# Optimization experiments

Measured on AMD Instinct MI355X. Metric: run time of the kernel, lower is better.

Reference implementation:

```python
import jax, jax.numpy as jnp
import numpy as np

N = 200000   # total nodes across batched graphs
E = 800000   # directed edges (grid graph, avg degree ~4)
G = 8        # number of graphs in the batch
IN_DIM, INTER_DIM, OUT_DIM, LAYER_NUM = 2, 128, 64, 4


def setup_inputs() -> dict:
    key = jax.random.key(0)
    ks = jax.random.split(key, 10)
    x = jax.random.normal(ks[0], (N, IN_DIM), jnp.float32)
    edge_index = jax.random.randint(ks[1], (2, E), 0, N, dtype=jnp.int32)
    batch = jnp.sort(jax.random.randint(ks[2], (N,), 0, G, dtype=jnp.int32))

    def glorot(k, fan_in, fan_out):
        s = (2.0 / (fan_in + fan_out)) ** 0.5
        return jax.random.normal(k, (fan_in, fan_out), jnp.float32) * s

    W_in = glorot(ks[3], IN_DIM, INTER_DIM)
    b_in = jnp.zeros((INTER_DIM,), jnp.float32)
    W_hidden = jnp.stack([glorot(jax.random.fold_in(ks[4], i), INTER_DIM, INTER_DIM)
                          for i in range(LAYER_NUM)])
    b_hidden = jnp.zeros((LAYER_NUM, INTER_DIM), jnp.float32)
    W_out = glorot(ks[5], INTER_DIM, OUT_DIM)
    b_out = jnp.zeros((OUT_DIM,), jnp.float32)
    return {"x": x, "edge_index": edge_index, "batch": batch,
            "W_in": W_in, "b_in": b_in, "W_hidden": W_hidden,
            "b_hidden": b_hidden, "W_out": W_out, "b_out": b_out}


def reference(x, edge_index, batch, W_in, b_in, W_hidden, b_hidden, W_out, b_out):
    num_nodes = x.shape[0]
    loops = jnp.arange(num_nodes, dtype=edge_index.dtype)
    # PyG GCNConv: add self loops, symmetric degree normalization
    src = jnp.concatenate([edge_index[0], loops])
    dst = jnp.concatenate([edge_index[1], loops])
    deg = jax.ops.segment_sum(jnp.ones_like(src, x.dtype), dst, num_segments=num_nodes)
    dinv = jnp.where(deg > 0, jax.lax.rsqrt(jnp.maximum(deg, 1.0)), 0.0)
    norm = dinv[src] * dinv[dst]  # [E+N]

    def gcn_conv(h, W, b):
        m = h @ W                                  # [N, F'] dense transform
        msg = norm[:, None] * m[src]               # gather + scale
        out = jax.ops.segment_sum(msg, dst, num_segments=num_nodes)  # scatter-add
        return out + b

    h = gcn_conv(x, W_in, b_in)
    for i in range(W_hidden.shape[0]):
        h = jax.nn.relu(gcn_conv(h, W_hidden[i], b_hidden[i]))
    h = gcn_conv(h, W_out, b_out)

    # global mean pool over batch assignment, then sigmoid
    sums = jax.ops.segment_sum(h, batch, num_segments=G)
    cnts = jax.ops.segment_sum(jnp.ones((num_nodes,), h.dtype), batch, num_segments=G)
    return jax.nn.sigmoid(sums / jnp.maximum(cnts, 1.0)[:, None])
```

## Files before the change

kernel.cpp:

```cpp
#include <hip/hip_runtime.h>
#include <math.h>

#define INTER 128
#define OUTD  64
#define SCAN_T 256
#define SCAN_E 1024
#define NSLOT 64
#define NBIN  128

using bf16x8 = __attribute__((ext_vector_type(8))) short;
using f32x4  = __attribute__((ext_vector_type(4))) float;

static __device__ __forceinline__ unsigned short f2bf(float f) {
    unsigned int u = __float_as_uint(f);
    u += 0x7fffu + ((u >> 16) & 1u);
    return (unsigned short)(u >> 16);
}
static __device__ __forceinline__ unsigned int pk2(float a, float b) {
    return (unsigned int)f2bf(a) | ((unsigned int)f2bf(b) << 16);
}
static __device__ __forceinline__ float bflo(unsigned int u) { return __uint_as_float(u << 16); }
static __device__ __forceinline__ float bfhi(unsigned int u) { return __uint_as_float(u & 0xffff0000u); }

static __device__ __forceinline__ void fma8(float* a, float w, uint4 v) {
    a[0] = fmaf(w, bflo(v.x), a[0]); a[1] = fmaf(w, bfhi(v.x), a[1]);
    a[2] = fmaf(w, bflo(v.y), a[2]); a[3] = fmaf(w, bfhi(v.y), a[3]);
    a[4] = fmaf(w, bflo(v.z), a[4]); a[5] = fmaf(w, bfhi(v.z), a[5]);
    a[6] = fmaf(w, bflo(v.w), a[6]); a[7] = fmaf(w, bfhi(v.w), a[7]);
}
static __device__ __forceinline__ void seed8(float* a, float sn, uint4 v) {
    a[0] = sn * bflo(v.x); a[1] = sn * bfhi(v.x);
    a[2] = sn * bflo(v.y); a[3] = sn * bfhi(v.y);
    a[4] = sn * bflo(v.z); a[5] = sn * bfhi(v.z);
    a[6] = sn * bflo(v.w); a[7] = sn * bfhi(v.w);
}

__global__ void count_k(const int* __restrict__ dst, int* __restrict__ cnt, int E) {
    int e = blockIdx.x * 256 + threadIdx.x;
    if (e < E) atomicAdd(&cnt[dst[e]], 1);
}

__global__ void dinv_k(const int* __restrict__ cnt, float* __restrict__ dinv, int N) {
    int i = blockIdx.x * 256 + threadIdx.x;
    if (i < N) dinv[i] = rsqrtf((float)(cnt[i] + 1));
}

__global__ void scan_block(const int* __restrict__ in, int* __restrict__ out,
                           int* __restrict__ bsums, int n) {
    __shared__ int sh[SCAN_T];
    int base = blockIdx.x * SCAN_E;
    int t = threadIdx.x;
    int v[4];
    int s = 0;
#pragma unroll
    for (int i = 0; i < 4; i++) {
        int idx = base + t * 4 + i;
        v[i] = (idx < n) ? in[idx] : 0;
        s += v[i];
    }
    sh[t] = s;
    __syncthreads();
    for (int off = 1; off < SCAN_T; off <<= 1) {
        int x = (t >= off) ? sh[t - off] : 0;
        __syncthreads();
        sh[t] += x;
        __syncthreads();
    }
    int excl = (t == 0) ? 0 : sh[t - 1];
    if (bsums && t == SCAN_T - 1) bsums[blockIdx.x] = sh[t];
#pragma unroll
    for (int i = 0; i < 4; i++) {
        int idx = base + t * 4 + i;
        if (idx < n) out[idx] = excl;
        excl += v[i];
    }
}

__global__ void scan_add(int* __restrict__ out, const int* __restrict__ bsums, int n, int total) {
    int idx = blockIdx.x * SCAN_E + threadIdx.x * 4;
    int add = bsums[blockIdx.x];
#pragma unroll
    for (int i = 0; i < 4; i++) {
        int j = idx + i;
        if (j < n) out[j] += add;
    }
    if (blockIdx.x == 0 && threadIdx.x == 0) out[n] = total;
}

__global__ void scatter_k(const int* __restrict__ src, const int* __restrict__ dst,
                          const int* __restrict__ rs, int* __restrict__ cursor,
                          const float* __restrict__ dinv,
                          int2* __restrict__ cw, int E) {
    int e = blockIdx.x * 256 + threadIdx.x;
    if (e >= E) return;
    int s = src[e], d = dst[e];
    int pos = rs[d] + atomicAdd(&cursor[d], 1);
    cw[pos] = make_int2(s, __float_as_int(dinv[s] * dinv[d]));
}

__global__ __launch_bounds__(256) void dhist2_k(const int* __restrict__ cnt,
                                                int* __restrict__ blockhist,
                                                int N, int nblk) {
    __shared__ int hist[NBIN];
    int t = threadIdx.x;
    if (t < NBIN) hist[t] = 0;
    __syncthreads();
    int i = blockIdx.x * 256 + t;
    if (i < N) atomicAdd(&hist[min(cnt[i], NBIN - 1)], 1);
    __syncthreads();
    if (t < NBIN) blockhist[t * nblk + blockIdx.x] = hist[t];
}

__global__ __launch_bounds__(256) void dorder2_k(const int* __restrict__ cnt,
                                                 const int* __restrict__ offs,
                                                 int* __restrict__ order,
                                                 int N, int nblk) {
    __shared__ int cur[NBIN];
    int t = threadIdx.x;
    if (t < NBIN) cur[t] = 0;
    __syncthreads();
    int i = blockIdx.x * 256 + t;
    if (i >= N) return;
    int d = min(cnt[i], NBIN - 1);
    int r = atomicAdd(&cur[d], 1);
    order[offs[d * nblk + blockIdx.x] + r] = i;
}

__global__ void wprep_h(const float* __restrict__ W, unsigned short* __restrict__ Wt, int L) {
    int tid = blockIdx.x * 256 + threadIdx.x;
    if (tid >= L * INTER * INTER) return;
    int l = tid / (INTER * INTER);
    int r = tid % (INTER * INTER);
    int n = r / INTER, k = r % INTER;
    Wt[tid] = f2bf(W[(size_t)l * INTER * INTER + (size_t)k * INTER + n]);
}

__global__ void wprep_o(const float* __restrict__ W, unsigned short* __restrict__ Wt) {
    int tid = blockIdx.x * 256 + threadIdx.x;
    if (tid >= OUTD * INTER) return;
    int n = tid / INTER, k = tid % INTER;
    Wt[tid] = f2bf(W[(size_t)k * OUTD + n]);
}

__global__ void agg2(const float* __restrict__ x, const int* __restrict__ rs,
                     const int2* __restrict__ cw, const float* __restrict__ dinv,
                     float* __restrict__ ax, int N) {
    int i = blockIdx.x * 256 + threadIdx.x;
    if (i >= N) return;
    float di = dinv[i];
    float sn = di * di;
    float2 xv = ((const float2*)x)[i];
    float a0 = sn * xv.x, a1 = sn * xv.y;
    int e0 = rs[i], e1 = rs[i + 1];
    for (int k = e0; k < e1; k++) {
        int2 c = cw[k];
        float wk = __int_as_float(c.y);
        float2 xs = ((const float2*)x)[c.x];
        a0 += wk * xs.x;
        a1 += wk * xs.y;
    }
    ((float2*)ax)[i] = make_float2(a0, a1);
}

__global__ void gemm_in(const float* __restrict__ ax, const float* __restrict__ Wi,
                        const float* __restrict__ bi, unsigned short* __restrict__ h, int N) {
    int node = blockIdx.x * 2 + threadIdx.x / 128;
    int j = threadIdx.x % 128;
    if (node >= N) return;
    float2 a = ((const float2*)ax)[node];
    h[(size_t)node * 128 + j] = f2bf(fmaf(a.x, Wi[j], fmaf(a.y, Wi[128 + j], bi[j])));
}

__global__ __launch_bounds__(256) void fused_hidden4(
    const unsigned short* __restrict__ Hin,
    const int* __restrict__ rs, const int2* __restrict__ cw,
    const float* __restrict__ dinv, const int* __restrict__ order,
    const unsigned short* __restrict__ Wt,
    const float* __restrict__ bias,
    unsigned short* __restrict__ Hout, int N)
{
    __shared__ __align__(16) unsigned short T[32][136];
    __shared__ int nodeid[32];
    const int t = threadIdx.x;
    const int q = t & 15;
    const int gi = t >> 4;
    const int sA = blockIdx.x * 32 + gi;
    const int sB = sA + 16;
    const bool vA = sA < N, vB = sB < N;
    const int nA = vA ? order[sA] : 0;
    const int nB = vB ? order[sB] : 0;
    if (q == 0) {
        nodeid[gi]      = vA ? nA : -1;
        nodeid[gi + 16] = vB ? nB : -1;
    }

    float accA[8] = {0,0,0,0,0,0,0,0}, accB[8] = {0,0,0,0,0,0,0,0};
    if (vA) {
        float dA = dinv[nA];
        seed8(accA, dA * dA, *(const uint4*)(Hin + (size_t)nA * 128 + q * 8));
    }
    if (vB) {
        float dB = dinv[nB];
        seed8(accB, dB * dB, *(const uint4*)(Hin + (size_t)nB * 128 + q * 8));
    }
    int kA = 0, eA = 0, kB = 0, eB = 0;
    if (vA) { kA = rs[nA]; eA = rs[nA + 1]; }
    if (vB) { kB = rs[nB]; eB = rs[nB + 1]; }

    while (kA < eA || kB < eB) {
        int2 cA0 = (kA     < eA) ? cw[kA]     : make_int2(0, 0);
        int2 cA1 = (kA + 1 < eA) ? cw[kA + 1] : make_int2(0, 0);
        int2 cA2 = (kA + 2 < eA) ? cw[kA + 2] : make_int2(0, 0);
        int2 cA3 = (kA + 3 < eA) ? cw[kA + 3] : make_int2(0, 0);
        int2 cB0 = (kB     < eB) ? cw[kB]     : make_int2(0, 0);
        int2 cB1 = (kB + 1 < eB) ? cw[kB + 1] : make_int2(0, 0);
        int2 cB2 = (kB + 2 < eB) ? cw[kB + 2] : make_int2(0, 0);
        int2 cB3 = (kB + 3 < eB) ? cw[kB + 3] : make_int2(0, 0);
        uint4 vA0 = *(const uint4*)(Hin + (size_t)cA0.x * 128 + q * 8);
        uint4 vA1 = *(const uint4*)(Hin + (size_t)cA1.x * 128 + q * 8);
        uint4 vA2 = *(const uint4*)(Hin + (size_t)cA2.x * 128 + q * 8);
        uint4 vA3 = *(const uint4*)(Hin + (size_t)cA3.x * 128 + q * 8);
        uint4 vB0 = *(const uint4*)(Hin + (size_t)cB0.x * 128 + q * 8);
        uint4 vB1 = *(const uint4*)(Hin + (size_t)cB1.x * 128 + q * 8);
        uint4 vB2 = *(const uint4*)(Hin + (size_t)cB2.x * 128 + q * 8);
        uint4 vB3 = *(const uint4*)(Hin + (size_t)cB3.x * 128 + q * 8);
        fma8(accA, __int_as_float(cA0.y), vA0);
        fma8(accA, __int_as_float(cA1.y), vA1);
        fma8(accA, __int_as_float(cA2.y), vA2);
        fma8(accA, __int_as_float(cA3.y), vA3);
        fma8(accB, __int_as_float(cB0.y), vB0);
        fma8(accB, __int_as_float(cB1.y), vB1);
        fma8(accB, __int_as_float(cB2.y), vB2);
        fma8(accB, __int_as_float(cB3.y), vB3);
        kA += 4; kB += 4;
    }

    {
        uint4 oA = make_uint4(pk2(accA[0], accA[1]), pk2(accA[2], accA[3]),
                              pk2(accA[4], accA[5]), pk2(accA[6], accA[7]));
        uint4 oB = make_uint4(pk2(accB[0], accB[1]), pk2(accB[2], accB[3]),
                              pk2(accB[4], accB[5]), pk2(accB[6], accB[7]));
        *(uint4*)&T[gi][q * 8] = oA;
        *(uint4*)&T[gi + 16][q * 8] = oB;
    }
    __syncthreads();

    const int wv = t >> 6;
    const int lane = t & 63;
    const int r15 = lane & 15;
    const int kg = lane >> 4;

    bf16x8 bfr[2][4];
#pragma unroll
    for (int nc = 0; nc < 2; nc++)
#pragma unroll
        for (int ks = 0; ks < 4; ks++)
            bfr[nc][ks] = *(const bf16x8*)&T[nc * 16 + r15][kg * 8 + ks * 32];

    f32x4 acc[2][2];
#pragma unroll
    for (int nc = 0; nc < 2; nc++)
#pragma unroll
        for (int c = 0; c < 2; c++) acc[nc][c] = (f32x4){0.f, 0.f, 0.f, 0.f};

#pragma unroll
    for (int c = 0; c < 2; c++) {
        const unsigned short* wrow = Wt + (size_t)(wv * 32 + c * 16 + r15) * 128 + kg * 8;
#pragma unroll
        for (int ks = 0; ks < 4; ks++) {
            bf16x8 afr = *(const bf16x8*)(wrow + ks * 32);
            acc[0][c] = __builtin_amdgcn_mfma_f32_16x16x32_bf16(afr, bfr[0][ks], acc[0][c], 0, 0, 0);
            acc[1][c] = __builtin_amdgcn_mfma_f32_16x16x32_bf16(afr, bfr[1][ks], acc[1][c], 0, 0, 0);
        }
    }

#pragma unroll
    for (int nc = 0; nc < 2; nc++) {
        const int node = nodeid[nc * 16 + r15];
        if (node >= 0) {
#pragma unroll
            for (int c = 0; c < 2; c++) {
                int col = wv * 32 + c * 16 + kg * 4;
                float4 bv = *(const float4*)(bias + col);
                float v0 = fmaxf(acc[nc][c][0] + bv.x, 0.f);
                float v1 = fmaxf(acc[nc][c][1] + bv.y, 0.f);
                float v2 = fmaxf(acc[nc][c][2] + bv.z, 0.f);
                float v3 = fmaxf(acc[nc][c][3] + bv.w, 0.f);
                *(uint2*)(Hout + (size_t)node * 128 + col) = make_uint2(pk2(v0, v1), pk2(v2, v3));
            }
        }
    }
}

__global__ __launch_bounds__(256) void gemm_out(const unsigned short* __restrict__ Hin,
                                                const unsigned short* __restrict__ Wt,
                                                unsigned short* __restrict__ g, int N) {
    const int wv = threadIdx.x >> 6;
    const int lane = threadIdx.x & 63;
    const int r15 = lane & 15;
    const int kg = lane >> 4;
    const int node0 = blockIdx.x * 64 + wv * 16;
    if (node0 >= N) return;

    int arow = node0 + r15;
    if (arow >= N) arow = N - 1;
    bf16x8 bfr[4];
#pragma unroll
    for (int ks = 0; ks < 4; ks++)
        bfr[ks] = __builtin_nontemporal_load(
            (const bf16x8*)(Hin + (size_t)arow * 128 + kg * 8 + ks * 32));

    f32x4 acc[4];
#pragma unroll
    for (int c = 0; c < 4; c++) acc[c] = (f32x4){0.f, 0.f, 0.f, 0.f};

#pragma unroll
    for (int c = 0; c < 4; c++) {
        const unsigned short* wrow = Wt + (size_t)(c * 16 + r15) * 128 + kg * 8;
#pragma unroll
        for (int ks = 0; ks < 4; ks++) {
            bf16x8 afr = *(const bf16x8*)(wrow + ks * 32);
            acc[c] = __builtin_amdgcn_mfma_f32_16x16x32_bf16(afr, bfr[ks], acc[c], 0, 0, 0);
        }
    }
    const int node = node0 + r15;
    if (node < N) {
#pragma unroll
        for (int c = 0; c < 4; c++) {
            int col = c * 16 + kg * 4;
            *(uint2*)(g + (size_t)node * 64 + col) =
                make_uint2(pk2(acc[c][0], acc[c][1]), pk2(acc[c][2], acc[c][3]));
        }
    }
}

__global__ __launch_bounds__(256) void fused_last2(
    const unsigned short* __restrict__ g,
    const int* __restrict__ rs, const int2* __restrict__ cw,
    const float* __restrict__ dinv, const int* __restrict__ batch,
    float* __restrict__ gsum , int N)
{
    __shared__ __align__(16) float R[64][68];
    __shared__ int gid[64];
    const int t = threadIdx.x;
    const int q = t & 7;
    const int gi = t >> 3;
    const int nA = blockIdx.x * 64 + gi;
    const int nB = nA + 32;
    const bool vA = nA < N, vB = nB < N;

    float accA[8] = {0,0,0,0,0,0,0,0}, accB[8] = {0,0,0,0,0,0,0,0};
    if (vA) {
        float dA = dinv[nA];
        seed8(accA, dA * dA, *(const uint4*)(g + (size_t)nA * 64 + q * 8));
    }
    if (vB) {
        float dB = dinv[nB];
        seed8(accB, dB * dB, *(const uint4*)(g + (size_t)nB * 64 + q * 8));
    }
    int kA = 0, eA = 0, kB = 0, eB = 0;
    if (vA) { kA = rs[nA]; eA = rs[nA + 1]; }
    if (vB) { kB = rs[nB]; eB = rs[nB + 1]; }

    while (kA < eA || kB < eB) {
        int2 cA0 = (kA     < eA) ? cw[kA]     : make_int2(0, 0);
        int2 cA1 = (kA + 1 < eA) ? cw[kA + 1] : make_int2(0, 0);
        int2 cA2 = (kA + 2 < eA) ? cw[kA + 2] : make_int2(0, 0);
        int2 cA3 = (kA + 3 < eA) ? cw[kA + 3] : make_int2(0, 0);
        int2 cB0 = (kB     < eB) ? cw[kB]     : make_int2(0, 0);
        int2 cB1 = (kB + 1 < eB) ? cw[kB + 1] : make_int2(0, 0);
        int2 cB2 = (kB + 2 < eB) ? cw[kB + 2] : make_int2(0, 0);
        int2 cB3 = (kB + 3 < eB) ? cw[kB + 3] : make_int2(0, 0);
        uint4 vA0 = *(const uint4*)(g + (size_t)cA0.x * 64 + q * 8);
        uint4 vA1 = *(const uint4*)(g + (size_t)cA1.x * 64 + q * 8);
        uint4 vA2 = *(const uint4*)(g + (size_t)cA2.x * 64 + q * 8);
        uint4 vA3 = *(const uint4*)(g + (size_t)cA3.x * 64 + q * 8);
        uint4 vB0 = *(const uint4*)(g + (size_t)cB0.x * 64 + q * 8);
        uint4 vB1 = *(const uint4*)(g + (size_t)cB1.x * 64 + q * 8);
        uint4 vB2 = *(const uint4*)(g + (size_t)cB2.x * 64 + q * 8);
        uint4 vB3 = *(const uint4*)(g + (size_t)cB3.x * 64 + q * 8);
        fma8(accA, __int_as_float(cA0.y), vA0);
        fma8(accA, __int_as_float(cA1.y), vA1);
        fma8(accA, __int_as_float(cA2.y), vA2);
        fma8(accA, __int_as_float(cA3.y), vA3);
        fma8(accB, __int_as_float(cB0.y), vB0);
        fma8(accB, __int_as_float(cB1.y), vB1);
        fma8(accB, __int_as_float(cB2.y), vB2);
        fma8(accB, __int_as_float(cB3.y), vB3);
        kA += 4; kB += 4;
    }

#pragma unroll
    for (int j = 0; j < 8; j += 4) {
        *(float4*)&R[gi][q * 8 + j]      = make_float4(accA[j], accA[j+1], accA[j+2], accA[j+3]);
        *(float4*)&R[gi + 32][q * 8 + j] = make_float4(accB[j], accB[j+1], accB[j+2], accB[j+3]);
    }
    if (q == 0) {
        gid[gi]      = vA ? batch[nA] : -1;
        gid[gi + 32] = vB ? batch[nB] : -1;
    }
    __syncthreads();

    const int f = t & 63;
    const int half = t >> 6;
    const int slot = blockIdx.x & (NSLOT - 1);
    float acc = 0.f;
    int cur = -1;
    for (int r = 0; r < 16; r++) {
        int row = half * 16 + r;
        int gg = gid[row];
        if (gg != cur) {
            if (cur >= 0) atomicAdd(&gsum[(size_t)(slot * 8 + cur) * 64 + f], acc);
            acc = 0.f; cur = gg;
        }
        if (gg >= 0) acc += R[row][f];
    }
    if (cur >= 0) atomicAdd(&gsum[(size_t)(slot * 8 + cur) * 64 + f], acc);
}

__global__ void gbound_k(const int* __restrict__ batch, int* __restrict__ gstart, int N, int G) {
    int i = blockIdx.x * 256 + threadIdx.x;
    if (i >= N) return;
    int b = batch[i];
    int prev = (i == 0) ? -1 : batch[i - 1];
    for (int g = prev + 1; g <= b; g++) gstart[g] = i;
    if (i == N - 1) for (int g = b + 1; g <= G; g++) gstart[g] = N;
}

__global__ void final4_k(const float* __restrict__ gsum, const int* __restrict__ gstart,
                         const float* __restrict__ b_out, float* __restrict__ out) {
    int t = threadIdx.x;
    int g = t >> 6, f = t & 63;
    float s = 0.f;
    for (int sl = 0; sl < NSLOT; sl++) s += gsum[(size_t)(sl * 8 + g) * 64 + f];
    int c = gstart[g + 1] - gstart[g];
    float v = s / (float)max(c, 1) + b_out[f];
    out[g * 64 + f] = 1.f / (1.f + expf(-v));
}

extern "C" void kernel_launch(void* const* d_in, const int* in_sizes, int n_in,
                              void* d_out, int out_size, void* d_ws, size_t ws_size,
                              hipStream_t stream) {
    const float* x     = (const float*)d_in[0];
    const int*   ei    = (const int*)d_in[1];
    const int*   batch = (const int*)d_in[2];
    const float* W_in  = (const float*)d_in[3];
    const float* b_in  = (const float*)d_in[4];
    const float* W_h   = (const float*)d_in[5];
    const float* b_h   = (const float*)d_in[6];
    const float* W_out = (const float*)d_in[7];
    const float* b_out = (const float*)d_in[8];

    const int N = in_sizes[2];
    const int E = in_sizes[1] / 2;
    const int L = in_sizes[5] / (INTER * INTER);
    const int G = 8;
    const int* src = ei;
    const int* dst = ei + E;
    const int nblk = (N + 255) / 256;
    const int nbh = NBIN * nblk;

    char* ws = (char*)d_ws;
    size_t off = 0;
    auto alloc = [&](size_t bytes) -> void* {
        void* p = ws + off;
        off += (bytes + 255) & ~(size_t)255;
        return p;
    };
    int*   cnt    = (int*)alloc((size_t)N * 4);
    int*   cursor = (int*)alloc((size_t)N * 4);
    int*   rs     = (int*)alloc((size_t)(N + 1) * 4);
    int*   bsums  = (int*)alloc(4096);
    float* dinv   = (float*)alloc((size_t)N * 4);
    int2*  cw     = (int2*)alloc((size_t)E * 8);
    float* ax     = (float*)alloc((size_t)N * 2 * 4);
    unsigned short* h   = (unsigned short*)alloc((size_t)N * INTER * 2);
    unsigned short* h2  = (unsigned short*)alloc((size_t)N * INTER * 2);
    unsigned short* g   = (unsigned short*)alloc((size_t)N * OUTD * 2);
    unsigned short* Wht = (unsigned short*)alloc((size_t)L * INTER * INTER * 2);
    unsigned short* Wot = (unsigned short*)alloc((size_t)OUTD * INTER * 2);
    float* gsum   = (float*)alloc((size_t)NSLOT * 8 * OUTD * 4);
    int*   gstart = (int*)alloc((G + 1) * 4);
    int*   bh     = (int*)alloc((size_t)(nbh + 1) * 4);
    int*   order  = (int*)alloc((size_t)N * 4);
    (void)ws_size; (void)n_in;

    hipMemsetAsync(cnt, 0, (size_t)N * 4, stream);
    hipMemsetAsync(cursor, 0, (size_t)N * 4, stream);
    hipMemsetAsync(gsum, 0, (size_t)NSLOT * 8 * OUTD * 4, stream);

    count_k<<<(E + 255) / 256, 256, 0, stream>>>(dst, cnt, E);
    dinv_k<<<nblk, 256, 0, stream>>>(cnt, dinv, N);
    int nsb = (N + SCAN_E - 1) / SCAN_E;
    scan_block<<<nsb, SCAN_T, 0, stream>>>(cnt, rs, bsums, N);
    scan_block<<<1, SCAN_T, 0, stream>>>(bsums, bsums, nullptr, nsb);
    scan_add<<<nsb, SCAN_T, 0, stream>>>(rs, bsums, N, E);
    scatter_k<<<(E + 255) / 256, 256, 0, stream>>>(src, dst, rs, cursor, dinv, cw, E);
    gbound_k<<<nblk, 256, 0, stream>>>(batch, gstart, N, G);

    dhist2_k<<<nblk, 256, 0, stream>>>(cnt, bh, N, nblk);
    int nsb2 = (nbh + SCAN_E - 1) / SCAN_E;
    scan_block<<<nsb2, SCAN_T, 0, stream>>>(bh, bh, bsums, nbh);
    scan_block<<<1, SCAN_T, 0, stream>>>(bsums, bsums, nullptr, nsb2);
    scan_add<<<nsb2, SCAN_T, 0, stream>>>(bh, bsums, nbh, N);
    dorder2_k<<<nblk, 256, 0, stream>>>(cnt, bh, order, N, nblk);

    wprep_h<<<(L * INTER * INTER + 255) / 256, 256, 0, stream>>>(W_h, Wht, L);
    wprep_o<<<(OUTD * INTER + 255) / 256, 256, 0, stream>>>(W_out, Wot);

    agg2<<<nblk, 256, 0, stream>>>(x, rs, cw, dinv, ax, N);
    gemm_in<<<(N + 1) / 2, 256, 0, stream>>>(ax, W_in, b_in, h, N);

    unsigned short* hin = h;
    unsigned short* hout = h2;
    for (int l = 0; l < L; l++) {
        fused_hidden4<<<(N + 31) / 32, 256, 0, stream>>>(
            hin, rs, cw, dinv, order, Wht + (size_t)l * INTER * INTER, b_h + (size_t)l * INTER, hout, N);
        unsigned short* tmp = hin; hin = hout; hout = tmp;
    }

    gemm_out<<<(N + 63) / 64, 256, 0, stream>>>(hin, Wot, g, N);
    fused_last2<<<(N + 63) / 64, 256, 0, stream>>>(g, rs, cw, dinv, batch, gsum, N);
    final4_k<<<1, 512, 0, stream>>>(gsum, gstart, b_out, (float*)d_out);
}
```

Before: 542.9 us.

## Fuse preprocessing kernels, pack per-node metadata, sort by graph and degree, deepen gather unroll

Merges dinv, graph-boundary and histogram kernels into one prep kernel, merges both weight-prep kernels, and fuses the input aggregation with the input linear layer. Nodes are now sorted by (graph, capped degree) into an int4 record holding node id, row range and dinv, so the hidden and last layers read one record instead of several scattered lookups. The hidden-layer gather unroll is raised from 4 to 8 edges per iteration for more memory-level parallelism, at the cost of more registers. The last layer now walks sorted order, which should make its pooled rows more graph-coherent. The two count/cursor memsets are merged into one, which assumes cursor sits right after cnt.

```diff
diff --git a/kernel.cpp b/kernel.cpp
--- a/kernel.cpp
+++ b/kernel.cpp
@@ -6,7 +6,7 @@
 #define SCAN_T 256
 #define SCAN_E 1024
 #define NSLOT 64
-#define NBIN  128
+#define NBIN  256
 
 using bf16x8 = __attribute__((ext_vector_type(8))) short;
 using f32x4  = __attribute__((ext_vector_type(4))) float;
@@ -38,11 +38,6 @@
 __global__ void count_k(const int* __restrict__ dst, int* __restrict__ cnt, int E) {
     int e = blockIdx.x * 256 + threadIdx.x;
     if (e < E) atomicAdd(&cnt[dst[e]], 1);
-}
-
-__global__ void dinv_k(const int* __restrict__ cnt, float* __restrict__ dinv, int N) {
-    int i = blockIdx.x * 256 + threadIdx.x;
-    if (i < N) dinv[i] = rsqrtf((float)(cnt[i] + 1));
 }
 
 __global__ void scan_block(const int* __restrict__ in, int* __restrict__ out,
@@ -98,22 +93,36 @@
     cw[pos] = make_int2(s, __float_as_int(dinv[s] * dinv[d]));
 }
 
-__global__ __launch_bounds__(256) void dhist2_k(const int* __restrict__ cnt,
-                                                int* __restrict__ blockhist,
-                                                int N, int nblk) {
+__global__ __launch_bounds__(256) void prep2_k(const int* __restrict__ cnt,
+                                               const int* __restrict__ batch,
+                                               float* __restrict__ dinv,
+                                               int* __restrict__ blockhist,
+                                               int* __restrict__ gstart,
+                                               int N, int G, int nblk) {
     __shared__ int hist[NBIN];
     int t = threadIdx.x;
     if (t < NBIN) hist[t] = 0;
     __syncthreads();
     int i = blockIdx.x * 256 + t;
-    if (i < N) atomicAdd(&hist[min(cnt[i], NBIN - 1)], 1);
+    if (i < N) {
+        int d = cnt[i];
+        dinv[i] = rsqrtf((float)(d + 1));
+        int b = batch[i];
+        atomicAdd(&hist[b * 32 + min(d, 31)], 1);
+        int prev = (i == 0) ? -1 : batch[i - 1];
+        for (int g2 = prev + 1; g2 <= b; g2++) gstart[g2] = i;
+        if (i == N - 1) for (int g2 = b + 1; g2 <= G; g2++) gstart[g2] = N;
+    }
     __syncthreads();
     if (t < NBIN) blockhist[t * nblk + blockIdx.x] = hist[t];
 }
 
-__global__ __launch_bounds__(256) void dorder2_k(const int* __restrict__ cnt,
+__global__ __launch_bounds__(256) void dorder3_k(const int* __restrict__ cnt,
+                                                 const int* __restrict__ batch,
+                                                 const int* __restrict__ rs,
+                                                 const float* __restrict__ dinv,
                                                  const int* __restrict__ offs,
-                                                 int* __restrict__ order,
+                                                 int4* __restrict__ srt,
                                                  int N, int nblk) {
     __shared__ int cur[NBIN];
     int t = threadIdx.x;
@@ -121,60 +130,87 @@
     __syncthreads();
     int i = blockIdx.x * 256 + t;
     if (i >= N) return;
-    int d = min(cnt[i], NBIN - 1);
-    int r = atomicAdd(&cur[d], 1);
-    order[offs[d * nblk + blockIdx.x] + r] = i;
-}
-
-__global__ void wprep_h(const float* __restrict__ W, unsigned short* __restrict__ Wt, int L) {
+    int key = batch[i] * 32 + min(cnt[i], 31);
+    int r = atomicAdd(&cur[key], 1);
+    int p = offs[key * nblk + blockIdx.x] + r;
+    srt[p] = make_int4(i, rs[i], rs[i + 1], __float_as_int(dinv[i]));
+}
+
+__global__ void wprep_all(const float* __restrict__ Wh, const float* __restrict__ Wo,
+                          unsigned short* __restrict__ Wht, unsigned short* __restrict__ Wot,
+                          int L) {
     int tid = blockIdx.x * 256 + threadIdx.x;
-    if (tid >= L * INTER * INTER) return;
-    int l = tid / (INTER * INTER);
-    int r = tid % (INTER * INTER);
-    int n = r / INTER, k = r % INTER;
-    Wt[tid] = f2bf(W[(size_t)l * INTER * INTER + (size_t)k * INTER + n]);
-}
-
-__global__ void wprep_o(const float* __restrict__ W, unsigned short* __restrict__ Wt) {
-    int tid = blockIdx.x * 256 + threadIdx.x;
-    if (tid >= OUTD * INTER) return;
-    int n = tid / INTER, k = tid % INTER;
-    Wt[tid] = f2bf(W[(size_t)k * OUTD + n]);
-}
-
-__global__ void agg2(const float* __restrict__ x, const int* __restrict__ rs,
-                     const int2* __restrict__ cw, const float* __restrict__ dinv,
-                     float* __restrict__ ax, int N) {
-    int i = blockIdx.x * 256 + threadIdx.x;
-    if (i >= N) return;
-    float di = dinv[i];
-    float sn = di * di;
-    float2 xv = ((const float2*)x)[i];
-    float a0 = sn * xv.x, a1 = sn * xv.y;
-    int e0 = rs[i], e1 = rs[i + 1];
-    for (int k = e0; k < e1; k++) {
-        int2 c = cw[k];
-        float wk = __int_as_float(c.y);
-        float2 xs = ((const float2*)x)[c.x];
-        a0 += wk * xs.x;
-        a1 += wk * xs.y;
-    }
-    ((float2*)ax)[i] = make_float2(a0, a1);
-}
-
-__global__ void gemm_in(const float* __restrict__ ax, const float* __restrict__ Wi,
-                        const float* __restrict__ bi, unsigned short* __restrict__ h, int N) {
-    int node = blockIdx.x * 2 + threadIdx.x / 128;
-    int j = threadIdx.x % 128;
-    if (node >= N) return;
-    float2 a = ((const float2*)ax)[node];
-    h[(size_t)node * 128 + j] = f2bf(fmaf(a.x, Wi[j], fmaf(a.y, Wi[128 + j], bi[j])));
-}
-
-__global__ __launch_bounds__(256) void fused_hidden4(
+    int nh = L * INTER * INTER;
+    if (tid < nh) {
+        int l = tid / (INTER * INTER);
+        int r = tid % (INTER * INTER);
+        int n = r / INTER, k = r % INTER;
+        Wht[tid] = f2bf(Wh[(size_t)l * INTER * INTER + (size_t)k * INTER + n]);
+    } else if (tid < nh + OUTD * INTER) {
+        int r = tid - nh;
+        int n = r / INTER, k = r % INTER;
+        Wot[r] = f2bf(Wo[(size_t)k * OUTD + n]);
+    }
+}
+
+__global__ __launch_bounds__(256) void agg_in_k(const float* __restrict__ x,
+                                                const int* __restrict__ rs,
+                                                const int2* __restrict__ cw,
+                                                const float* __restrict__ dinv,
+                                                const float* __restrict__ Wi,
+                                                const float* __restrict__ bi,
+                                                unsigned short* __restrict__ h, int N) {
+    __shared__ float2 axs[256];
+    int t = threadIdx.x;
+    int i = blockIdx.x * 256 + t;
+    float a0 = 0.f, a1 = 0.f;
+    if (i < N) {
+        float di = dinv[i];
+        float sn = di * di;
+        float2 xv = ((const float2*)x)[i];
+        a0 = sn * xv.x; a1 = sn * xv.y;
+        int e0 = rs[i], e1 = rs[i + 1];
+        for (int k = e0; k < e1; k += 2) {
+            int2 c0 = cw[k];
+            int2 c1 = (k + 1 < e1) ? cw[k + 1] : make_int2(0, 0);
+            float2 x0 = ((const float2*)x)[c0.x];
+            float2 x1 = ((const float2*)x)[c1.x];
+            float w0 = __int_as_float(c0.y), w1 = __int_as_float(c1.y);
+            a0 = fmaf(w0, x0.x, a0); a1 = fmaf(w0, x0.y, a1);
+            a0 = fmaf(w1, x1.x, a0); a1 = fmaf(w1, x1.y, a1);
+        }
+    }
+    axs[t] = make_float2(a0, a1);
+    __syncthreads();
+    int base = blockIdx.x * 256;
+#pragma unroll
+    for (int p = 0; p < 16; p++) {
+        int nl = p * 16 + (t >> 4);
+        int nb = base + nl;
+        if (nb < N) {
+            int j0 = (t & 15) * 8;
+            float2 a = axs[nl];
+            float4 wa0 = *(const float4*)&Wi[j0];       float4 wa1 = *(const float4*)&Wi[j0 + 4];
+            float4 wb0 = *(const float4*)&Wi[128 + j0]; float4 wb1 = *(const float4*)&Wi[128 + j0 + 4];
+            float4 bb0 = *(const float4*)&bi[j0];       float4 bb1 = *(const float4*)&bi[j0 + 4];
+            float h0 = fmaf(a.x, wa0.x, fmaf(a.y, wb0.x, bb0.x));
+            float h1 = fmaf(a.x, wa0.y, fmaf(a.y, wb0.y, bb0.y));
+            float h2 = fmaf(a.x, wa0.z, fmaf(a.y, wb0.z, bb0.z));
+            float h3 = fmaf(a.x, wa0.w, fmaf(a.y, wb0.w, bb0.w));
+            float h4 = fmaf(a.x, wa1.x, fmaf(a.y, wb1.x, bb1.x));
+            float h5 = fmaf(a.x, wa1.y, fmaf(a.y, wb1.y, bb1.y));
+            float h6 = fmaf(a.x, wa1.z, fmaf(a.y, wb1.z, bb1.z));
+            float h7 = fmaf(a.x, wa1.w, fmaf(a.y, wb1.w, bb1.w));
+            *(uint4*)(h + (size_t)nb * 128 + j0) =
+                make_uint4(pk2(h0, h1), pk2(h2, h3), pk2(h4, h5), pk2(h6, h7));
+        }
+    }
+}
+
+__global__ __launch_bounds__(256) void fused_hidden6(
     const unsigned short* __restrict__ Hin,
-    const int* __restrict__ rs, const int2* __restrict__ cw,
-    const float* __restrict__ dinv, const int* __restrict__ order,
+    const int2* __restrict__ cw,
+    const int4* __restrict__ srt,
     const unsigned short* __restrict__ Wt,
     const float* __restrict__ bias,
     unsigned short* __restrict__ Hout, int N)
@@ -186,53 +222,45 @@
     const int gi = t >> 4;
     const int sA = blockIdx.x * 32 + gi;
     const int sB = sA + 16;
-    const bool vA = sA < N, vB = sB < N;
-    const int nA = vA ? order[sA] : 0;
-    const int nB = vB ? order[sB] : 0;
+    int4 dA = (sA < N) ? srt[sA] : make_int4(-1, 0, 0, 0);
+    int4 dB = (sB < N) ? srt[sB] : make_int4(-1, 0, 0, 0);
     if (q == 0) {
-        nodeid[gi]      = vA ? nA : -1;
-        nodeid[gi + 16] = vB ? nB : -1;
+        nodeid[gi]      = dA.x;
+        nodeid[gi + 16] = dB.x;
     }
 
     float accA[8] = {0,0,0,0,0,0,0,0}, accB[8] = {0,0,0,0,0,0,0,0};
-    if (vA) {
-        float dA = dinv[nA];
-        seed8(accA, dA * dA, *(const uint4*)(Hin + (size_t)nA * 128 + q * 8));
-    }
-    if (vB) {
-        float dB = dinv[nB];
-        seed8(accB, dB * dB, *(const uint4*)(Hin + (size_t)nB * 128 + q * 8));
-    }
     int kA = 0, eA = 0, kB = 0, eB = 0;
-    if (vA) { kA = rs[nA]; eA = rs[nA + 1]; }
-    if (vB) { kB = rs[nB]; eB = rs[nB + 1]; }
+    if (dA.x >= 0) {
+        float dv = __int_as_float(dA.w);
+        seed8(accA, dv * dv, *(const uint4*)(Hin + (size_t)dA.x * 128 + q * 8));
+        kA = dA.y; eA = dA.z;
+    }
+    if (dB.x >= 0) {
+        float dv = __int_as_float(dB.w);
+        seed8(accB, dv * dv, *(const uint4*)(Hin + (size_t)dB.x * 128 + q * 8));
+        kB = dB.y; eB = dB.z;
+    }
 
     while (kA < eA || kB < eB) {
-        int2 cA0 = (kA     < eA) ? cw[kA]     : make_int2(0, 0);
-        int2 cA1 = (kA + 1 < eA) ? cw[kA + 1] : make_int2(0, 0);
-        int2 cA2 = (kA + 2 < eA) ? cw[kA + 2] : make_int2(0, 0);
-        int2 cA3 = (kA + 3 < eA) ? cw[kA + 3] : make_int2(0, 0);
-        int2 cB0 = (kB     < eB) ? cw[kB]     : make_int2(0, 0);
-        int2 cB1 = (kB + 1 < eB) ? cw[kB + 1] : make_int2(0, 0);
-        int2 cB2 = (kB + 2 < eB) ? cw[kB + 2] : make_int2(0, 0);
-        int2 cB3 = (kB + 3 < eB) ? cw[kB + 3] : make_int2(0, 0);
-        uint4 vA0 = *(const uint4*)(Hin + (size_t)cA0.x * 128 + q * 8);
-        uint4 vA1 = *(const uint4*)(Hin + (size_t)cA1.x * 128 + q * 8);
-        uint4 vA2 = *(const uint4*)(Hin + (size_t)cA2.x * 128 + q * 8);
-        uint4 vA3 = *(const uint4*)(Hin + (size_t)cA3.x * 128 + q * 8);
-        uint4 vB0 = *(const uint4*)(Hin + (size_t)cB0.x * 128 + q * 8);
-        uint4 vB1 = *(const uint4*)(Hin + (size_t)cB1.x * 128 + q * 8);
-        uint4 vB2 = *(const uint4*)(Hin + (size_t)cB2.x * 128 + q * 8);
-        uint4 vB3 = *(const uint4*)(Hin + (size_t)cB3.x * 128 + q * 8);
-        fma8(accA, __int_as_float(cA0.y), vA0);
-        fma8(accA, __int_as_float(cA1.y), vA1);
-        fma8(accA, __int_as_float(cA2.y), vA2);
-        fma8(accA, __int_as_float(cA3.y), vA3);
-        fma8(accB, __int_as_float(cB0.y), vB0);
-        fma8(accB, __int_as_float(cB1.y), vB1);
-        fma8(accB, __int_as_float(cB2.y), vB2);
-        fma8(accB, __int_as_float(cB3.y), vB3);
-        kA += 4; kB += 4;
+        int2 cA[8], cB[8];
+#pragma unroll
+        for (int u = 0; u < 8; u++) {
+            cA[u] = (kA + u < eA) ? cw[kA + u] : make_int2(0, 0);
+            cB[u] = (kB + u < eB) ? cw[kB + u] : make_int2(0, 0);
+        }
+        uint4 vA[8], vB[8];
+#pragma unroll
+        for (int u = 0; u < 8; u++) {
+            vA[u] = *(const uint4*)(Hin + (size_t)cA[u].x * 128 + q * 8);
+            vB[u] = *(const uint4*)(Hin + (size_t)cB[u].x * 128 + q * 8);
+        }
+#pragma unroll
+        for (int u = 0; u < 8; u++) {
+            fma8(accA, __int_as_float(cA[u].y), vA[u]);
+            fma8(accB, __int_as_float(cB[u].y), vB[u]);
+        }
+        kA += 8; kB += 8;
     }
 
     {
@@ -334,10 +362,11 @@
     }
 }
 
-__global__ __launch_bounds__(256) void fused_last2(
+__global__ __launch_bounds__(256) void fused_last3(
     const unsigned short* __restrict__ g,
-    const int* __restrict__ rs, const int2* __restrict__ cw,
-    const float* __restrict__ dinv, const int* __restrict__ batch,
+    const int2* __restrict__ cw,
+    const int4* __restrict__ srt,
+    const int* __restrict__ batch,
     float* __restrict__ gsum , int N)
 {
     __shared__ __align__(16) float R[64][68];
@@ -345,48 +374,46 @@
     const int t = threadIdx.x;
     const int q = t & 7;
     const int gi = t >> 3;
-    const int nA = blockIdx.x * 64 + gi;
-    const int nB = nA + 32;
-    const bool vA = nA < N, vB = nB < N;
+    const int sA = blockIdx.x * 64 + gi;
+    const int sB = sA + 32;
+    int4 dA = (sA < N) ? srt[sA] : make_int4(-1, 0, 0, 0);
+    int4 dB = (sB < N) ? srt[sB] : make_int4(-1, 0, 0, 0);
+    if (q == 0) {
+        gid[gi]      = (dA.x >= 0) ? batch[dA.x] : -1;
+        gid[gi + 32] = (dB.x >= 0) ? batch[dB.x] : -1;
+    }
 
     float accA[8] = {0,0,0,0,0,0,0,0}, accB[8] = {0,0,0,0,0,0,0,0};
-    if (vA) {
-        float dA = dinv[nA];
-        seed8(accA, dA * dA, *(const uint4*)(g + (size_t)nA * 64 + q * 8));
-    }
-    if (vB) {
-        float dB = dinv[nB];
-        seed8(accB, dB * dB, *(const uint4*)(g + (size_t)nB * 64 + q * 8));
-    }
     int kA = 0, eA = 0, kB = 0, eB = 0;
-    if (vA) { kA = rs[nA]; eA = rs[nA + 1]; }
-    if (vB) { kB = rs[nB]; eB = rs[nB + 1]; }
+    if (dA.x >= 0) {
+        float dv = __int_as_float(dA.w);
+        seed8(accA, dv * dv, *(const uint4*)(g + (size_t)dA.x * 64 + q * 8));
+        kA = dA.y; eA = dA.z;
+    }
+    if (dB.x >= 0) {
+        float dv = __int_as_float(dB.w);
+        seed8(accB, dv * dv, *(const uint4*)(g + (size_t)dB.x * 64 + q * 8));
+        kB = dB.y; eB = dB.z;
+    }
 
     while (kA < eA || kB < eB) {
-        int2 cA0 = (kA     < eA) ? cw[kA]     : make_int2(0, 0);
-        int2 cA1 = (kA + 1 < eA) ? cw[kA + 1] : make_int2(0, 0);
-        int2 cA2 = (kA + 2 < eA) ? cw[kA + 2] : make_int2(0, 0);
-        int2 cA3 = (kA + 3 < eA) ? cw[kA + 3] : make_int2(0, 0);
-        int2 cB0 = (kB     < eB) ? cw[kB]     : make_int2(0, 0);
-        int2 cB1 = (kB + 1 < eB) ? cw[kB + 1] : make_int2(0, 0);
-        int2 cB2 = (kB + 2 < eB) ? cw[kB + 2] : make_int2(0, 0);
-        int2 cB3 = (kB + 3 < eB) ? cw[kB + 3] : make_int2(0, 0);
-        uint4 vA0 = *(const uint4*)(g + (size_t)cA0.x * 64 + q * 8);
-        uint4 vA1 = *(const uint4*)(g + (size_t)cA1.x * 64 + q * 8);
-        uint4 vA2 = *(const uint4*)(g + (size_t)cA2.x * 64 + q * 8);
-        uint4 vA3 = *(const uint4*)(g + (size_t)cA3.x * 64 + q * 8);
-        uint4 vB0 = *(const uint4*)(g + (size_t)cB0.x * 64 + q * 8);
-        uint4 vB1 = *(const uint4*)(g + (size_t)cB1.x * 64 + q * 8);
-        uint4 vB2 = *(const uint4*)(g + (size_t)cB2.x * 64 + q * 8);
-        uint4 vB3 = *(const uint4*)(g + (size_t)cB3.x * 64 + q * 8);
-        fma8(accA, __int_as_float(cA0.y), vA0);
-        fma8(accA, __int_as_float(cA1.y), vA1);
-        fma8(accA, __int_as_float(cA2.y), vA2);
-        fma8(accA, __int_as_float(cA3.y), vA3);
-        fma8(accB, __int_as_float(cB0.y), vB0);
-        fma8(accB, __int_as_float(cB1.y), vB1);
-        fma8(accB, __int_as_float(cB2.y), vB2);
-        fma8(accB, __int_as_float(cB3.y), vB3);
+        int2 cA[4], cB[4];
+#pragma unroll
+        for (int u = 0; u < 4; u++) {
+            cA[u] = (kA + u < eA) ? cw[kA + u] : make_int2(0, 0);
+            cB[u] = (kB + u < eB) ? cw[kB + u] : make_int2(0, 0);
+        }
+        uint4 vA[4], vB[4];
+#pragma unroll
+        for (int u = 0; u < 4; u++) {
+            vA[u] = *(const uint4*)(g + (size_t)cA[u].x * 64 + q * 8);
+            vB[u] = *(const uint4*)(g + (size_t)cB[u].x * 64 + q * 8);
+        }
+#pragma unroll
+        for (int u = 0; u < 4; u++) {
+            fma8(accA, __int_as_float(cA[u].y), vA[u]);
+            fma8(accB, __int_as_float(cB[u].y), vB[u]);
+        }
         kA += 4; kB += 4;
     }
 
@@ -394,10 +421,6 @@
     for (int j = 0; j < 8; j += 4) {
         *(float4*)&R[gi][q * 8 + j]      = make_float4(accA[j], accA[j+1], accA[j+2], accA[j+3]);
         *(float4*)&R[gi + 32][q * 8 + j] = make_float4(accB[j], accB[j+1], accB[j+2], accB[j+3]);
-    }
-    if (q == 0) {
-        gid[gi]      = vA ? batch[nA] : -1;
-        gid[gi + 32] = vB ? batch[nB] : -1;
     }
     __syncthreads();
 
@@ -416,15 +439,6 @@
         if (gg >= 0) acc += R[row][f];
     }
     if (cur >= 0) atomicAdd(&gsum[(size_t)(slot * 8 + cur) * 64 + f], acc);
-}
-
-__global__ void gbound_k(const int* __restrict__ batch, int* __restrict__ gstart, int N, int G) {
-    int i = blockIdx.x * 256 + threadIdx.x;
-    if (i >= N) return;
-    int b = batch[i];
-    int prev = (i == 0) ? -1 : batch[i - 1];
-    for (int g = prev + 1; g <= b; g++) gstart[g] = i;
-    if (i == N - 1) for (int g = b + 1; g <= G; g++) gstart[g] = N;
 }
 
 __global__ void final4_k(const float* __restrict__ gsum, const int* __restrict__ gstart,
@@ -473,7 +487,6 @@
     int*   bsums  = (int*)alloc(4096);
     float* dinv   = (float*)alloc((size_t)N * 4);
     int2*  cw     = (int2*)alloc((size_t)E * 8);
-    float* ax     = (float*)alloc((size_t)N * 2 * 4);
     unsigned short* h   = (unsigned short*)alloc((size_t)N * INTER * 2);
     unsigned short* h2  = (unsigned short*)alloc((size_t)N * INTER * 2);
     unsigned short* g   = (unsigned short*)alloc((size_t)N * OUTD * 2);
@@ -482,44 +495,40 @@
     float* gsum   = (float*)alloc((size_t)NSLOT * 8 * OUTD * 4);
     int*   gstart = (int*)alloc((G + 1) * 4);
     int*   bh     = (int*)alloc((size_t)(nbh + 1) * 4);
-    int*   order  = (int*)alloc((size_t)N * 4);
+    int4*  srt    = (int4*)alloc((size_t)N * 16);
     (void)ws_size; (void)n_in;
 
-    hipMemsetAsync(cnt, 0, (size_t)N * 4, stream);
-    hipMemsetAsync(cursor, 0, (size_t)N * 4, stream);
+    hipMemsetAsync(cnt, 0, (size_t)N * 8, stream);
     hipMemsetAsync(gsum, 0, (size_t)NSLOT * 8 * OUTD * 4, stream);
 
     count_k<<<(E + 255) / 256, 256, 0, stream>>>(dst, cnt, E);
-    dinv_k<<<nblk, 256, 0, stream>>>(cnt, dinv, N);
     int nsb = (N + SCAN_E - 1) / SCAN_E;
     scan_block<<<nsb, SCAN_T, 0, stream>>>(cnt, rs, bsums, N);
     scan_block<<<1, SCAN_T, 0, stream>>>(bsums, bsums, nullptr, nsb);
     scan_add<<<nsb, SCAN_T, 0, stream>>>(rs, bsums, N, E);
+    prep2_k<<<nblk, 256, 0, stream>>>(cnt, batch, dinv, bh, gstart, N, G, nblk);
     scatter_k<<<(E + 255) / 256, 256, 0, stream>>>(src, dst, rs, cursor, dinv, cw, E);
-    gbound_k<<<nblk, 256, 0, stream>>>(batch, gstart, N, G);
-
-    dhist2_k<<<nblk, 256, 0, stream>>>(cnt, bh, N, nblk);
+
     int nsb2 = (nbh + SCAN_E - 1) / SCAN_E;
     scan_block<<<nsb2, SCAN_T, 0, stream>>>(bh, bh, bsums, nbh);
     scan_block<<<1, SCAN_T, 0, stream>>>(bsums, bsums, nullptr, nsb2);
     scan_add<<<nsb2, SCAN_T, 0, stream>>>(bh, bsums, nbh, N);
-    dorder2_k<<<nblk, 256, 0, stream>>>(cnt, bh, order, N, nblk);
-
-    wprep_h<<<(L * INTER * INTER + 255) / 256, 256, 0, stream>>>(W_h, Wht, L);
-    wprep_o<<<(OUTD * INTER + 255) / 256, 256, 0, stream>>>(W_out, Wot);
-
-    agg2<<<nblk, 256, 0, stream>>>(x, rs, cw, dinv, ax, N);
-    gemm_in<<<(N + 1) / 2, 256, 0, stream>>>(ax, W_in, b_in, h, N);
+    dorder3_k<<<nblk, 256, 0, stream>>>(cnt, batch, rs, dinv, bh, srt, N, nblk);
+
+    int wtot = L * INTER * INTER + OUTD * INTER;
+    wprep_all<<<(wtot + 255) / 256, 256, 0, stream>>>(W_h, W_out, Wht, Wot, L);
+
+    agg_in_k<<<nblk, 256, 0, stream>>>(x, rs, cw, dinv, W_in, b_in, h, N);
 
     unsigned short* hin = h;
     unsigned short* hout = h2;
     for (int l = 0; l < L; l++) {
-        fused_hidden4<<<(N + 31) / 32, 256, 0, stream>>>(
-            hin, rs, cw, dinv, order, Wht + (size_t)l * INTER * INTER, b_h + (size_t)l * INTER, hout, N);
+        fused_hidden6<<<(N + 31) / 32, 256, 0, stream>>>(
+            hin, cw, srt, Wht + (size_t)l * INTER * INTER, b_h + (size_t)l * INTER, hout, N);
         unsigned short* tmp = hin; hin = hout; hout = tmp;
     }
 
     gemm_out<<<(N + 63) / 64, 256, 0, stream>>>(hin, Wot, g, N);
-    fused_last2<<<(N + 63) / 64, 256, 0, stream>>>(g, rs, cw, dinv, batch, gsum, N);
+    fused_last3<<<(N + 63) / 64, 256, 0, stream>>>(g, cw, srt, batch, gsum, N);
     final4_k<<<1, 512, 0, stream>>>(gsum, gstart, b_out, (float*)d_out);
 }
```

New measurement: 594.5 us. 9.5% more time.
